# Kernel optimization log

Hardware: AMD Instinct MI355X
Metric: run time of the kernel (lower is better)

Reference implementation:

```python
import jax, jax.numpy as jnp
import numpy as np

D = 512
CELLS = 16
BATCH = 4
SEQ = 1024


def setup_inputs() -> dict:
    key = jax.random.key(0)
    ks = jax.random.split(key, 5)
    x = jax.random.normal(ks[0], (BATCH * CELLS, SEQ, D), dtype=jnp.float32)
    # causal mask: True where attention is disallowed (strict upper triangle)
    m = ~jnp.tril(jnp.ones((SEQ, SEQ), dtype=bool))
    gamma = jnp.ones((D,), dtype=jnp.float32)
    beta = jnp.zeros((D,), dtype=jnp.float32)
    Wg = jax.random.normal(ks[1], (D, D), dtype=jnp.float32) * (D ** -0.5)
    inhibit = jax.random.normal(ks[2], (CELLS, CELLS), dtype=jnp.float32) * 0.02
    phases = jnp.linspace(0.0, 2.0 * np.pi, CELLS, dtype=jnp.float32)
    res_scale = jnp.ones((1,), dtype=jnp.float32) * 0.1
    return {"x": x, "m": m, "gamma": gamma, "beta": beta, "Wg": Wg,
            "inhibit": inhibit, "phases": phases, "res_scale": res_scale,
            "B": BATCH, "T": SEQ}


def _layernorm(x, gamma, beta, eps=1e-5):
    mu = jnp.mean(x, axis=-1, keepdims=True)
    var = jnp.var(x, axis=-1, keepdims=True)
    return (x - mu) * jax.lax.rsqrt(var + eps) * gamma + beta


def reference(x, m, gamma, beta, Wg, inhibit, phases, res_scale, B, T):
    d = x.shape[-1]
    cells = inhibit.shape[0]
    nx = _layernorm(x, gamma, beta)
    qkv = nx @ Wg.T                                  # [BC, T, d]
    att = jnp.einsum('bqd,bkd->bqk', qkv, qkv) * (d ** -0.5)  # [BC, T, T]
    att = jnp.where(m, -jnp.inf, att)
    x = x + jax.nn.softmax(att, axis=-1) @ qkv       # [BC, T, d]
    sync = x.reshape(B, cells, T, d)
    competed = jnp.einsum('bctd,ck->bktd', sync, inhibit)
    pulse = jnp.sin(competed + phases[None, :, None, None])
    return x + pulse.reshape(B * cells, T, d) * res_scale
```

## Files before the change

### kernel.cpp

```cpp
#include <hip/hip_runtime.h>
#include <stdint.h>

#define TSEQ 1024
#define DDIM 512

typedef __attribute__((ext_vector_type(8))) short bf16x8;
typedef __attribute__((ext_vector_type(4))) float f32x4;

#define MFMA(a, b, c) __builtin_amdgcn_mfma_f32_16x16x32_bf16((a), (b), (c), 0, 0, 0)

__device__ __forceinline__ unsigned short f2bf(float f) {
  unsigned int u = __builtin_bit_cast(unsigned int, f);
  u += 0x7FFFu + ((u >> 16) & 1u);
  return (unsigned short)(u >> 16);
}

__device__ __forceinline__ void async_load16(const void* g, void* l) {
  __builtin_amdgcn_global_load_lds(
      (const __attribute__((address_space(1))) unsigned int*)g,
      (__attribute__((address_space(3))) unsigned int*)l, 16, 0, 0);
}

__global__ __launch_bounds__(256) void k_ln(const float* __restrict__ x,
                                            const float* __restrict__ gamma,
                                            const float* __restrict__ beta,
                                            unsigned short* __restrict__ nx) {
  const int wid = threadIdx.x >> 6, lane = threadIdx.x & 63;
  const long long row = (long long)blockIdx.x * 4 + wid;
  const float* xr = x + row * DDIM + lane * 8;
  float4 a = *(const float4*)xr;
  float4 b = *(const float4*)(xr + 4);
  float s = a.x + a.y + a.z + a.w + b.x + b.y + b.z + b.w;
  float s2 = a.x * a.x + a.y * a.y + a.z * a.z + a.w * a.w +
             b.x * b.x + b.y * b.y + b.z * b.z + b.w * b.w;
#pragma unroll
  for (int m = 1; m < 64; m <<= 1) {
    s += __shfl_xor(s, m);
    s2 += __shfl_xor(s2, m);
  }
  const float mu = s * (1.0f / DDIM);
  const float var = s2 * (1.0f / DDIM) - mu * mu;
  const float rsd = rsqrtf(var + 1e-5f);
  const float4 g0 = *(const float4*)(gamma + lane * 8);
  const float4 g1 = *(const float4*)(gamma + lane * 8 + 4);
  const float4 b0 = *(const float4*)(beta + lane * 8);
  const float4 b1 = *(const float4*)(beta + lane * 8 + 4);
  float o0 = (a.x - mu) * rsd * g0.x + b0.x;
  float o1 = (a.y - mu) * rsd * g0.y + b0.y;
  float o2 = (a.z - mu) * rsd * g0.z + b0.z;
  float o3 = (a.w - mu) * rsd * g0.w + b0.w;
  float o4 = (b.x - mu) * rsd * g1.x + b1.x;
  float o5 = (b.y - mu) * rsd * g1.y + b1.y;
  float o6 = (b.z - mu) * rsd * g1.z + b1.z;
  float o7 = (b.w - mu) * rsd * g1.w + b1.w;
  uint4 pk;
  pk.x = f2bf(o0) | ((unsigned)f2bf(o1) << 16);
  pk.y = f2bf(o2) | ((unsigned)f2bf(o3) << 16);
  pk.z = f2bf(o4) | ((unsigned)f2bf(o5) << 16);
  pk.w = f2bf(o6) | ((unsigned)f2bf(o7) << 16);
  *(uint4*)(nx + row * DDIM + lane * 8) = pk;
}

__global__ __launch_bounds__(256) void k_cast(const float* __restrict__ w,
                                              unsigned short* __restrict__ o, int n8) {
  const int i = blockIdx.x * 256 + threadIdx.x;
  if (i >= n8) return;
  const float4 a = *(const float4*)(w + (size_t)i * 8);
  const float4 b = *(const float4*)(w + (size_t)i * 8 + 4);
  uint4 pk;
  pk.x = f2bf(a.x) | ((unsigned)f2bf(a.y) << 16);
  pk.y = f2bf(a.z) | ((unsigned)f2bf(a.w) << 16);
  pk.z = f2bf(b.x) | ((unsigned)f2bf(b.y) << 16);
  pk.w = f2bf(b.z) | ((unsigned)f2bf(b.w) << 16);
  *(uint4*)(o + (size_t)i * 8) = pk;
}

__global__ __launch_bounds__(256, 2) void k_gemm(const unsigned short* __restrict__ A,
                                                 const unsigned short* __restrict__ B,
                                                 unsigned short* __restrict__ C,
                                                 unsigned short* __restrict__ W) {
  __shared__ char sbuf[33280];
  char* As = sbuf;
  char* Bs = sbuf + 16384;
  const int tid = threadIdx.x;
  const int wid = tid >> 6, lane = tid & 63;
  const int g = lane >> 4, c = lane & 15;
  const int wr = wid >> 1, wc = wid & 1;
  const int bm = blockIdx.y, bn = blockIdx.x;

  int srcoff[4], ldsoff[4];
#pragma unroll
  for (int r = 0; r < 4; ++r) {
    const int aoff = r * 4096 + tid * 16;
    srcoff[r] = (aoff >> 7) * 1024 + (aoff & 127);
    ldsoff[r] = r * 4096 + (wid << 10);
  }
  const char* Ab = (const char*)A + (size_t)bm * 131072;
  const char* Bb = (const char*)B + (size_t)bn * 131072;

  f32x4 acc[4][4] = {};

  for (int ks = 0; ks < 8; ++ks) {
    __syncthreads();
#pragma unroll
    for (int r = 0; r < 4; ++r) {
      async_load16(Ab + ks * 128 + srcoff[r], As + ldsoff[r]);
      async_load16(Bb + ks * 128 + srcoff[r], Bs + ldsoff[r]);
    }
    __syncthreads();
    bf16x8 af[4][2], bfr[4][2];
#pragma unroll
    for (int f = 0; f < 4; ++f) {
#pragma unroll
      for (int kk = 0; kk < 2; ++kk) {
        const int rowa = wr * 64 + f * 16 + c;
        af[f][kk] = *(const bf16x8*)(As + rowa * 128 + (kk * 4 + g) * 16);
        const int rowb = wc * 64 + f * 16 + c;
        bfr[f][kk] = *(const bf16x8*)(Bs + rowb * 128 + (kk * 4 + g) * 16);
      }
    }
#pragma unroll
    for (int i = 0; i < 4; ++i) {
#pragma unroll
      for (int j = 0; j < 4; ++j) {
        acc[i][j] = MFMA(af[i][0], bfr[j][0], acc[i][j]);
        acc[i][j] = MFMA(af[i][1], bfr[j][1], acc[i][j]);
      }
    }
  }

#pragma unroll
  for (int i = 0; i < 4; ++i) {
#pragma unroll
    for (int r = 0; r < 4; ++r) {
      const long long row = (long long)bm * 128 + wr * 64 + i * 16 + g * 4 + r;
#pragma unroll
      for (int j = 0; j < 4; ++j) {
        const int col = bn * 128 + wc * 64 + j * 16 + c;
        C[row * DDIM + col] = f2bf(acc[i][j][r]);
      }
    }
  }

  __syncthreads();
  unsigned short* tb = (unsigned short*)sbuf;
#pragma unroll
  for (int i = 0; i < 4; ++i)
#pragma unroll
    for (int j = 0; j < 4; ++j)
#pragma unroll
      for (int r = 0; r < 4; ++r)
        tb[(wr * 64 + i * 16 + g * 4 + r) * 130 + wc * 64 + j * 16 + c] =
            f2bf(acc[i][j][r]);
  __syncthreads();
  const int bc = bm >> 3;
  const int kvt = (bm & 7) * 4 + wid;
#pragma unroll
  for (int dt_l = 0; dt_l < 8; ++dt_l) {
    const int d_l = dt_l * 16 + c;
    const int kv0 = wid * 32 + g * 8;
    bf16x8 v;
#pragma unroll
    for (int j = 0; j < 8; ++j) v[j] = tb[(kv0 + j) * 130 + d_l];
    const size_t woff =
        ((((size_t)bc * 32 + kvt) * 32) + bn * 8 + dt_l) * 1024 + lane * 16;
    *(bf16x8*)((char*)W + woff) = v;
  }
}

__global__ __launch_bounds__(512, 2) void k_attn(const unsigned short* __restrict__ qkv,
                                                 const unsigned short* __restrict__ W,
                                                 const float* __restrict__ x,
                                                 float* __restrict__ xo) {
  __shared__ char lds[131072];
  const int tid = threadIdx.x;
  const int wid = tid >> 6, lane = tid & 63;
  const int g = lane >> 4, c = lane & 15;
  const int bc = blockIdx.x;
  const size_t bcbase = (size_t)bc * TSEQ * DDIM;
  const float K1 = 0.0637587155f;
  const float K2 = -11.5415603f;

  int e0[2], e1[2];
#pragma unroll
  for (int ft = 0; ft < 2; ++ft) {
    const int row = ((c >> 2) << 3) + (ft << 2) + (c & 3);
    const int kap = ((ft << 2) | (c & 3)) ^ ((c >> 2) << 1);
    e0[ft] = row * 1024 + ((g ^ kap) << 4);
    e1[ft] = row * 1024 + (((4 + g) ^ kap) << 4);
  }

  int soffK[4];
#pragma unroll
  for (int r = 0; r < 4; ++r) {
    const int row = wid * 4 + r;
    const int kap = (row & 7) ^ (((row >> 3) & 3) << 1);
    soffK[r] = row * 1024 + ((lane ^ kap) << 4);
  }
  const char* kgb = (const char*)(qkv + bcbase);
  const char* wtb = (const char*)W + ((size_t)bc << 20);

#pragma unroll 1
  for (int h = 0; h < 2; ++h) {
    const int qt = h == 0 ? 7 - blockIdx.y : blockIdx.y;
    const int qrow = qt * 128 + wid * 16 + c;
    const int wave_qmin = qt * 128 + wid * 16;
    const int NT = 4 * qt + 4;

    bf16x8 qf[16];
    const unsigned short* qp = qkv + bcbase + (size_t)qrow * DDIM + g * 8;
#pragma unroll
    for (int ks = 0; ks < 16; ++ks) qf[ks] = *(const bf16x8*)(qp + ks * 32);

    f32x4 oacc[32] = {};
    float lrun = 0.0f;

    {
      char* kb = lds;
      char* vb = lds + 65536;
#pragma unroll
      for (int r = 0; r < 4; ++r) {
        async_load16(kgb + soffK[r], kb + wid * 4096 + r * 1024 + lane * 16);
        async_load16(wtb + r * 8192 + tid * 16, vb + r * 8192 + (wid << 10));
      }
    }

    for (int kvt = 0; kvt < NT; ++kvt) {
      __syncthreads();
      const char* kb = lds + (kvt & 1) * 32768;
      const char* vb = lds + 65536 + (kvt & 1) * 32768;

      if (kvt + 1 < NT) {
        char* kd = lds + ((kvt + 1) & 1) * 32768;
        char* vd = lds + 65536 + ((kvt + 1) & 1) * 32768;
        const char* ksrc = kgb + (kvt + 1) * 32768;
        const char* vsrc = wtb + (size_t)(kvt + 1) * 32768;
#pragma unroll
        for (int r = 0; r < 4; ++r) {
          async_load16(ksrc + soffK[r], kd + wid * 4096 + r * 1024 + lane * 16);
          async_load16(vsrc + r * 8192 + tid * 16, vd + r * 8192 + (wid << 10));
        }
      }

      if (kvt * 32 > wave_qmin + 15) continue;

      f32x4 stA[2] = {}, stB[2] = {};
      __builtin_amdgcn_s_setprio(1);
#pragma unroll
      for (int ks = 0; ks < 8; ++ks) {
        const int imm = (ks >> 1) * 128;
#pragma unroll
        for (int ft = 0; ft < 2; ++ft) {
          const bf16x8 kf = *(const bf16x8*)(kb + imm + ((ks & 1) ? e1[ft] : e0[ft]));
          stA[ft] = MFMA(kf, qf[ks], stA[ft]);
        }
      }
#pragma unroll
      for (int ks = 8; ks < 16; ++ks) {
        const int imm = (ks >> 1) * 128;
#pragma unroll
        for (int ft = 0; ft < 2; ++ft) {
          const bf16x8 kf = *(const bf16x8*)(kb + imm + ((ks & 1) ? e1[ft] : e0[ft]));
          stB[ft] = MFMA(kf, qf[ks], stB[ft]);
        }
      }
      __builtin_amdgcn_s_setprio(0);
      f32x4 st[2];
      st[0] = stA[0] + stB[0];
      st[1] = stA[1] + stB[1];

      float ex[2][4];
      if (kvt * 32 + 31 <= wave_qmin) {
#pragma unroll
        for (int ft = 0; ft < 2; ++ft)
#pragma unroll
          for (int r = 0; r < 4; ++r)
            ex[ft][r] = exp2f(fmaf(st[ft][r], K1, K2));
      } else {
#pragma unroll
        for (int ft = 0; ft < 2; ++ft)
#pragma unroll
          for (int r = 0; r < 4; ++r) {
            const int kvg = kvt * 32 + g * 8 + ft * 4 + r;
            ex[ft][r] = (kvg > qrow) ? 0.0f : exp2f(fmaf(st[ft][r], K1, K2));
          }
      }
#pragma unroll
      for (int ft = 0; ft < 2; ++ft)
#pragma unroll
        for (int r = 0; r < 4; ++r) lrun += ex[ft][r];

      bf16x8 pa0;
#pragma unroll
      for (int r = 0; r < 4; ++r) {
        pa0[r] = (short)f2bf(ex[0][r]);
        pa0[r + 4] = (short)f2bf(ex[1][r]);
      }

      const char* vp = vb + lane * 16;
#pragma unroll
      for (int dt = 0; dt < 32; ++dt) {
        const bf16x8 b0 = *(const bf16x8*)(vp + dt * 1024);
        oacc[dt] = MFMA(pa0, b0, oacc[dt]);
      }
    }

    float lr = lrun;
    lr += __shfl_xor(lr, 16);
    lr += __shfl_xor(lr, 32);
    const float rl = 1.0f / lr;
    float rlr[4];
#pragma unroll
    for (int r = 0; r < 4; ++r) rlr[r] = __shfl(rl, g * 4 + r);
#pragma unroll
    for (int dt = 0; dt < 32; ++dt) {
#pragma unroll
      for (int r = 0; r < 4; ++r) {
        const size_t off =
            bcbase + (size_t)(qt * 128 + wid * 16 + g * 4 + r) * DDIM + dt * 16 + c;
        xo[off] = x[off] + oacc[dt][r] * rlr[r];
      }
    }
    __syncthreads();
  }
}

__global__ __launch_bounds__(256) void k_mix(float* __restrict__ xo,
                                             const float* __restrict__ inh,
                                             const float* __restrict__ phz,
                                             const float* __restrict__ rsc) {
  __shared__ float sI[256];
  __shared__ float sP[16];
  const int tid = threadIdx.x;
  sI[tid] = inh[tid];
  if (tid < 16) sP[tid] = phz[tid];
  __syncthreads();
  const float rs = rsc[0];
  const int idx = blockIdx.x * 256 + tid;
  const int d4 = idx & 127;
  const int t = (idx >> 7) & 1023;
  const int b = idx >> 17;
  float4* base = (float4*)xo + ((size_t)b * 16 * TSEQ + t) * 128 + d4;
  float4 v[16];
#pragma unroll
  for (int cc = 0; cc < 16; ++cc) v[cc] = base[(size_t)cc * TSEQ * 128];
#pragma unroll
  for (int k = 0; k < 16; ++k) {
    float4 comp = make_float4(0.f, 0.f, 0.f, 0.f);
#pragma unroll
    for (int cc = 0; cc < 16; ++cc) {
      const float w = sI[cc * 16 + k];
      comp.x += v[cc].x * w;
      comp.y += v[cc].y * w;
      comp.z += v[cc].z * w;
      comp.w += v[cc].w * w;
    }
    const float ph = sP[k];
    float4 o;
    o.x = v[k].x + __sinf(comp.x + ph) * rs;
    o.y = v[k].y + __sinf(comp.y + ph) * rs;
    o.z = v[k].z + __sinf(comp.z + ph) * rs;
    o.w = v[k].w + __sinf(comp.w + ph) * rs;
    base[(size_t)k * TSEQ * 128] = o;
  }
}

extern "C" void kernel_launch(void* const* d_in, const int* in_sizes, int n_in,
                              void* d_out, int out_size, void* d_ws, size_t ws_size,
                              hipStream_t stream) {
  const float* x = (const float*)d_in[0];
  const float* gamma = (const float*)d_in[2];
  const float* beta = (const float*)d_in[3];
  const float* Wg = (const float*)d_in[4];
  const float* inh = (const float*)d_in[5];
  const float* phz = (const float*)d_in[6];
  const float* rsc = (const float*)d_in[7];
  float* out = (float*)d_out;

  unsigned short* qkv = (unsigned short*)d_ws;
  unsigned short* W = qkv + (size_t)33554432;
  unsigned short* nx = (unsigned short*)d_out;
  unsigned short* wgb = (unsigned short*)((char*)d_out + 104857600);

  k_cast<<<128, 256, 0, stream>>>(Wg, wgb, 32768);
  k_ln<<<16384, 256, 0, stream>>>(x, gamma, beta, nx);
  k_gemm<<<dim3(4, 512), 256, 0, stream>>>(nx, wgb, qkv, W);
  k_attn<<<dim3(64, 4), 512, 0, stream>>>(qkv, W, x, out);
  k_mix<<<2048, 256, 0, stream>>>(out, inh, phz, rsc);
}
```

Before: 320.9 us.

## Repartition PV matmul so each wave owns a D-slice via shared-LDS P tile

The P·V stage is reorganised. Each wave now writes its bf16 softmax probabilities into a shared LDS tile, and after a block barrier it computes the output for all 8 query groups over its own 64-column slice of D, instead of all 512 columns for its own 16 rows. Each wave therefore reads only 4 V fragments per kv tile rather than 32, which cuts LDS read traffic for V. In exchange it adds an extra __syncthreads per kv tile, LDS traffic for P, more LDS use (which may affect the 2-blocks-per-CU occupancy target), and a shared denominator buffer for the final normalisation.

```diff
diff --git a/kernel.cpp b/kernel.cpp
--- a/kernel.cpp
+++ b/kernel.cpp
@@ -172,7 +172,9 @@
                                                  const unsigned short* __restrict__ W,
                                                  const float* __restrict__ x,
                                                  float* __restrict__ xo) {
-  __shared__ char lds[131072];
+  __shared__ char lds[139776];
+  char* Pb = lds + 131072;
+  float* ldenom = (float*)(lds + 139264);
   const int tid = threadIdx.x;
   const int wid = tid >> 6, lane = tid & 63;
   const int g = lane >> 4, c = lane & 15;
@@ -181,6 +183,8 @@
   const float K1 = 0.0637587155f;
   const float K2 = -11.5415603f;
 
+  const int poff = c * 64 + ((g ^ ((c >> 1) & 3)) << 4);
+
   int e0[2], e1[2];
 #pragma unroll
   for (int ft = 0; ft < 2; ++ft) {
@@ -212,7 +216,7 @@
 #pragma unroll
     for (int ks = 0; ks < 16; ++ks) qf[ks] = *(const bf16x8*)(qp + ks * 32);
 
-    f32x4 oacc[32] = {};
+    f32x4 oacc[8][4] = {};
     float lrun = 0.0f;
 
     {
@@ -242,83 +246,98 @@
         }
       }
 
-      if (kvt * 32 > wave_qmin + 15) continue;
-
-      f32x4 stA[2] = {}, stB[2] = {};
-      __builtin_amdgcn_s_setprio(1);
-#pragma unroll
-      for (int ks = 0; ks < 8; ++ks) {
-        const int imm = (ks >> 1) * 128;
-#pragma unroll
-        for (int ft = 0; ft < 2; ++ft) {
-          const bf16x8 kf = *(const bf16x8*)(kb + imm + ((ks & 1) ? e1[ft] : e0[ft]));
-          stA[ft] = MFMA(kf, qf[ks], stA[ft]);
-        }
-      }
-#pragma unroll
-      for (int ks = 8; ks < 16; ++ks) {
-        const int imm = (ks >> 1) * 128;
-#pragma unroll
-        for (int ft = 0; ft < 2; ++ft) {
-          const bf16x8 kf = *(const bf16x8*)(kb + imm + ((ks & 1) ? e1[ft] : e0[ft]));
-          stB[ft] = MFMA(kf, qf[ks], stB[ft]);
-        }
-      }
-      __builtin_amdgcn_s_setprio(0);
-      f32x4 st[2];
-      st[0] = stA[0] + stB[0];
-      st[1] = stA[1] + stB[1];
-
-      float ex[2][4];
-      if (kvt * 32 + 31 <= wave_qmin) {
+      if (kvt * 32 <= wave_qmin + 15) {
+        f32x4 stA[2] = {}, stB[2] = {};
+        __builtin_amdgcn_s_setprio(1);
+#pragma unroll
+        for (int ks = 0; ks < 8; ++ks) {
+          const int imm = (ks >> 1) * 128;
+#pragma unroll
+          for (int ft = 0; ft < 2; ++ft) {
+            const bf16x8 kf = *(const bf16x8*)(kb + imm + ((ks & 1) ? e1[ft] : e0[ft]));
+            stA[ft] = MFMA(kf, qf[ks], stA[ft]);
+          }
+        }
+#pragma unroll
+        for (int ks = 8; ks < 16; ++ks) {
+          const int imm = (ks >> 1) * 128;
+#pragma unroll
+          for (int ft = 0; ft < 2; ++ft) {
+            const bf16x8 kf = *(const bf16x8*)(kb + imm + ((ks & 1) ? e1[ft] : e0[ft]));
+            stB[ft] = MFMA(kf, qf[ks], stB[ft]);
+          }
+        }
+        __builtin_amdgcn_s_setprio(0);
+        f32x4 st[2];
+        st[0] = stA[0] + stB[0];
+        st[1] = stA[1] + stB[1];
+
+        float ex[2][4];
+        if (kvt * 32 + 31 <= wave_qmin) {
+#pragma unroll
+          for (int ft = 0; ft < 2; ++ft)
+#pragma unroll
+            for (int r = 0; r < 4; ++r)
+              ex[ft][r] = exp2f(fmaf(st[ft][r], K1, K2));
+        } else {
+#pragma unroll
+          for (int ft = 0; ft < 2; ++ft)
+#pragma unroll
+            for (int r = 0; r < 4; ++r) {
+              const int kvg = kvt * 32 + g * 8 + ft * 4 + r;
+              ex[ft][r] = (kvg > qrow) ? 0.0f : exp2f(fmaf(st[ft][r], K1, K2));
+            }
+        }
 #pragma unroll
         for (int ft = 0; ft < 2; ++ft)
 #pragma unroll
-          for (int r = 0; r < 4; ++r)
-            ex[ft][r] = exp2f(fmaf(st[ft][r], K1, K2));
-      } else {
-#pragma unroll
-        for (int ft = 0; ft < 2; ++ft)
-#pragma unroll
-          for (int r = 0; r < 4; ++r) {
-            const int kvg = kvt * 32 + g * 8 + ft * 4 + r;
-            ex[ft][r] = (kvg > qrow) ? 0.0f : exp2f(fmaf(st[ft][r], K1, K2));
-          }
-      }
-#pragma unroll
-      for (int ft = 0; ft < 2; ++ft)
-#pragma unroll
-        for (int r = 0; r < 4; ++r) lrun += ex[ft][r];
-
-      bf16x8 pa0;
-#pragma unroll
-      for (int r = 0; r < 4; ++r) {
-        pa0[r] = (short)f2bf(ex[0][r]);
-        pa0[r + 4] = (short)f2bf(ex[1][r]);
-      }
-
-      const char* vp = vb + lane * 16;
-#pragma unroll
-      for (int dt = 0; dt < 32; ++dt) {
-        const bf16x8 b0 = *(const bf16x8*)(vp + dt * 1024);
-        oacc[dt] = MFMA(pa0, b0, oacc[dt]);
+          for (int r = 0; r < 4; ++r) lrun += ex[ft][r];
+
+        bf16x8 pa0;
+#pragma unroll
+        for (int r = 0; r < 4; ++r) {
+          pa0[r] = (short)f2bf(ex[0][r]);
+          pa0[r + 4] = (short)f2bf(ex[1][r]);
+        }
+        *(bf16x8*)(Pb + wid * 1024 + poff) = pa0;
+      }
+
+      __syncthreads();
+
+      const char* vp = vb + (wid * 4) * 1024 + lane * 16;
+      const bf16x8 v0 = *(const bf16x8*)(vp);
+      const bf16x8 v1 = *(const bf16x8*)(vp + 1024);
+      const bf16x8 v2 = *(const bf16x8*)(vp + 2048);
+      const bf16x8 v3 = *(const bf16x8*)(vp + 3072);
+#pragma unroll
+      for (int qg = 0; qg < 8; ++qg) {
+        if (qt * 128 + qg * 16 + 15 >= kvt * 32) {
+          const bf16x8 pa = *(const bf16x8*)(Pb + qg * 1024 + poff);
+          oacc[qg][0] = MFMA(pa, v0, oacc[qg][0]);
+          oacc[qg][1] = MFMA(pa, v1, oacc[qg][1]);
+          oacc[qg][2] = MFMA(pa, v2, oacc[qg][2]);
+          oacc[qg][3] = MFMA(pa, v3, oacc[qg][3]);
+        }
       }
     }
 
     float lr = lrun;
     lr += __shfl_xor(lr, 16);
     lr += __shfl_xor(lr, 32);
-    const float rl = 1.0f / lr;
-    float rlr[4];
-#pragma unroll
-    for (int r = 0; r < 4; ++r) rlr[r] = __shfl(rl, g * 4 + r);
-#pragma unroll
-    for (int dt = 0; dt < 32; ++dt) {
+    if (lane < 16) ldenom[wid * 16 + lane] = 1.0f / lr;
+    __syncthreads();
+#pragma unroll
+    for (int qg = 0; qg < 8; ++qg) {
 #pragma unroll
       for (int r = 0; r < 4; ++r) {
-        const size_t off =
-            bcbase + (size_t)(qt * 128 + wid * 16 + g * 4 + r) * DDIM + dt * 16 + c;
-        xo[off] = x[off] + oacc[dt][r] * rlr[r];
+        const float rv = ldenom[qg * 16 + g * 4 + r];
+        const size_t rb =
+            bcbase + (size_t)(qt * 128 + qg * 16 + g * 4 + r) * DDIM + wid * 64 + c;
+#pragma unroll
+        for (int dtl = 0; dtl < 4; ++dtl) {
+          const size_t off = rb + dtl * 16;
+          xo[off] = x[off] + oacc[qg][dtl][r] * rv;
+        }
       }
     }
     __syncthreads();
```

Result: faster. 313.4 us (-2.3%).
